# Kernel optimization log

Measured on AMD Instinct MI355X. Metric: run time of the kernel, lower is better.

Reference implementation:

```python
import jax, jax.numpy as jnp
import numpy as np

BN_EPS = 1e-5


def conv1x1(x, w, b):
    # x: (B,C,H,W), w: (O,C), b: (O,)
    return jnp.einsum('bchw,oc->bohw', x, w) + b[None, :, None, None]


def maxpool2(x):
    # 2x2 max pool, stride 2; H,W assumed even
    B, C, H, W = x.shape
    return x.reshape(B, C, H // 2, 2, W // 2, 2).max(axis=(3, 5))


def setup_inputs() -> dict:
    key = jax.random.key(0)
    ks = jax.random.split(key, 8)
    B, C, Ci, H, W = 8, 256, 128, 64, 64
    s_in = 1.0 / np.sqrt(C)   # kaiming-uniform-ish scale for 1x1 convs
    s_ci = 1.0 / np.sqrt(Ci)
    return {
        'x': jax.random.normal(ks[0], (B, C, H, W), jnp.float32),
        'theta_w': jax.random.normal(ks[1], (Ci, C), jnp.float32) * s_in,
        'theta_b': jnp.zeros((Ci,), jnp.float32),
        'phi_w': jax.random.normal(ks[2], (Ci, C), jnp.float32) * s_in,
        'phi_b': jnp.zeros((Ci,), jnp.float32),
        'g_w': jax.random.normal(ks[3], (Ci, C), jnp.float32) * s_in,
        'g_b': jnp.zeros((Ci,), jnp.float32),
        'W_w': jax.random.normal(ks[4], (C, Ci), jnp.float32) * s_ci,
        'W_b': jnp.zeros((C,), jnp.float32),
        'bn_gamma': jnp.ones((C,), jnp.float32),
        'bn_beta': jnp.zeros((C,), jnp.float32),
    }


def reference(x, theta_w, theta_b, phi_w, phi_b, g_w, g_b, W_w, W_b, bn_gamma, bn_beta):
    B, C, H, W = x.shape
    Ci = theta_w.shape[0]
    # 1x1 conv projections
    theta = conv1x1(x, theta_w, theta_b).reshape(B, Ci, H * W)           # (B,Ci,N)
    phi = maxpool2(conv1x1(x, phi_w, phi_b)).reshape(B, Ci, -1)          # (B,Ci,M)
    g = maxpool2(conv1x1(x, g_w, g_b)).reshape(B, Ci, -1)                # (B,Ci,M)
    # attention: softmax(theta^T phi) g^T
    attn = jax.nn.softmax(jnp.einsum('bcn,bcm->bnm', theta, phi), axis=-1)  # (B,N,M)
    y = jnp.einsum('bnm,bcm->bcn', attn, g).reshape(B, Ci, H, W)
    # output projection + BatchNorm2d (training-mode batch stats) + residual
    y = conv1x1(y, W_w, W_b)
    mean = y.mean(axis=(0, 2, 3))
    var = y.var(axis=(0, 2, 3))
    y = (y - mean[None, :, None, None]) * jax.lax.rsqrt(var + BN_EPS)[None, :, None, None]
    y = y * bn_gamma[None, :, None, None] + bn_beta[None, :, None, None]
    return x + y
```

## Files before the change

kernel.cpp:

```cpp
#include <hip/hip_runtime.h>

#define B_ 8
#define C_ 256
#define CI_ 128
#define N_ 4096
#define M_ 1024

typedef unsigned short u16;
typedef unsigned int u32;
typedef _Float16 f16x8 __attribute__((ext_vector_type(8)));
typedef _Float16 f16x4 __attribute__((ext_vector_type(4)));
typedef float f32x4 __attribute__((ext_vector_type(4)));
typedef u16 u16x4 __attribute__((ext_vector_type(4)));
typedef u16 u16x8 __attribute__((ext_vector_type(8)));

__device__ __forceinline__ u16 f2h(float f) {
    _Float16 h = (_Float16)f;
    u16 u;
    __builtin_memcpy(&u, &h, 2);
    return u;
}
__device__ __forceinline__ float h2f(u16 u) {
    _Float16 h;
    __builtin_memcpy(&h, &u, 2);
    return (float)h;
}
__device__ __forceinline__ f16x8 ldh8(const u16* p) {
    return *reinterpret_cast<const f16x8*>(p);
}
__device__ __forceinline__ f32x4 MFMAH(f16x8 a, f16x8 b, f32x4 c) {
    return __builtin_amdgcn_mfma_f32_16x16x32_f16(a, b, c, 0, 0, 0);
}
__device__ __forceinline__ f32x4 MFMA16(f16x4 a, f16x4 b, f32x4 c) {
    return __builtin_amdgcn_mfma_f32_16x16x16f16(a, b, c, 0, 0, 0);
}
__device__ __forceinline__ void gld16(const u16* g, u16* l) {
    __builtin_amdgcn_global_load_lds(
        (const __attribute__((address_space(1))) void*)g,
        (__attribute__((address_space(3))) void*)l, 16, 0, 0);
}


__global__ __launch_bounds__(256) void k_prep(
    const float* __restrict__ tw, const float* __restrict__ tb,
    const float* __restrict__ pw, const float* __restrict__ pb,
    const float* __restrict__ gw, const float* __restrict__ gb,
    const float* __restrict__ Ww,
    u16* __restrict__ wcf, float* __restrict__ bcat, u16* __restrict__ wwf) {
    int idx = blockIdx.x * 256 + threadIdx.x;
    if (idx < 384 * 256) {
        int r = idx >> 8, c = idx & 255;
        float v = (r < 128) ? tw[r * 256 + c]
                : (r < 256) ? pw[(r - 128) * 256 + c]
                            : gw[(r - 256) * 256 + c];
        size_t off = (size_t)((r >> 4) * 8 + (c >> 5)) * 512 +
                     (((c >> 3) & 3) * 16 + (r & 15)) * 8 + (c & 7);
        wcf[off] = f2h(v);
    } else if (idx < 384 * 256 + 256 * 128) {
        int k2 = idx - 384 * 256;
        int c = k2 >> 7, k = k2 & 127;
        size_t off = (size_t)((c >> 4) * 4 + (k >> 5)) * 512 +
                     (((k >> 3) & 3) * 16 + (c & 15)) * 8 + (k & 7);
        wwf[off] = f2h(Ww[k2]);
    } else if (idx < 384 * 256 + 256 * 128 + 384) {
        int r = idx - (384 * 256 + 256 * 128);
        bcat[r] = (r < 128) ? tb[r] : (r < 256) ? pb[r - 128] : gb[r - 256];
    }
}

__global__ __launch_bounds__(256) void k_tx(const float* __restrict__ x,
                                            u16* __restrict__ xbf) {
    int bid = blockIdx.x;
    int b = bid >> 8, rem = bid & 255, nt = rem >> 2, ct = rem & 3;
    int n0 = nt * 64, c0 = ct * 64;
    __shared__ u16 th_[64][66];
    int j = threadIdx.x & 63, i0 = threadIdx.x >> 6;
    for (int i = i0; i < 64; i += 4)
        th_[i][j] = f2h(x[((size_t)b * C_ + c0 + i) * N_ + n0 + j]);
    __syncthreads();
    int w = threadIdx.x >> 6, lane = threadIdx.x & 63;
    int l15 = lane & 15, g16 = lane >> 4;
    int s = w;
#pragma unroll
    for (int kk = 0; kk < 2; ++kk) {
        u16x8 hv;
#pragma unroll
        for (int e = 0; e < 8; ++e)
            hv[e] = th_[kk * 32 + g16 * 8 + e][s * 16 + l15];
        size_t off = ((size_t)(b * 256 + (n0 >> 4) + s) * 8 + (c0 >> 5) + kk) * 512 +
                     (size_t)lane * 8;
        *(u16x8*)&xbf[off] = hv;
    }
}

__global__ __launch_bounds__(256) void k_proj(
    const u16* __restrict__ wcf, const float* __restrict__ bcat,
    const u16* __restrict__ xbf,
    u16* __restrict__ thf, u16* __restrict__ ppf, u16* __restrict__ gpf) {
    int bid = blockIdx.x;
    int b = bid / 96, rem = bid % 96, rt = rem >> 5, nt = rem & 31;
    int tid = threadIdx.x;
    int w = tid >> 6, lane = tid & 63;
    int l15 = lane & 15, g16 = lane >> 4;
    int wr = (w >> 1) * 64, wc = (w & 1) * 64;
    int rbase = rt * 128 + wr, nbase = nt * 128 + wc;
    __shared__ u16 tl[128][132];
    f32x4 acc[4][4];
#pragma unroll
    for (int i = 0; i < 4; ++i)
#pragma unroll
        for (int j = 0; j < 4; ++j)
#pragma unroll
            for (int r = 0; r < 4; ++r) acc[i][j][r] = 0.f;
#pragma unroll
    for (int ks = 0; ks < 8; ++ks) {
        f16x8 a[4], bb[4];
#pragma unroll
        for (int i = 0; i < 4; ++i)
            a[i] = ldh8(&wcf[((size_t)((rbase >> 4) + i) * 8 + ks) * 512 + (size_t)lane * 8]);
#pragma unroll
        for (int j = 0; j < 4; ++j)
            bb[j] = ldh8(&xbf[((size_t)(b * 256 + (nbase >> 4) + j) * 8 + ks) * 512 +
                              (size_t)lane * 8]);
#pragma unroll
        for (int i = 0; i < 4; ++i)
#pragma unroll
            for (int j = 0; j < 4; ++j) acc[i][j] = MFMAH(a[i], bb[j], acc[i][j]);
    }
    if (rt == 0) {
#pragma unroll
        for (int i = 0; i < 4; ++i) {
            int lrow = wr + i * 16 + g16 * 4;
#pragma unroll
            for (int j = 0; j < 4; ++j) {
                u16x4 pk;
#pragma unroll
                for (int r = 0; r < 4; ++r)
                    pk[r] = f2h(acc[i][j][r] + bcat[lrow + r]);
                size_t off = ((size_t)(b * 256 + (nbase >> 4) + j) * 4 + (lrow >> 5)) * 512 +
                             (((lrow >> 3) & 3) * 16 + l15) * 8 + (lrow & 7);
                *reinterpret_cast<u16x4*>(&thf[off]) = pk;
            }
        }
    } else {
#pragma unroll
        for (int i = 0; i < 4; ++i) {
            int lrow = wr + i * 16 + g16 * 4;
#pragma unroll
            for (int j = 0; j < 4; ++j) {
                int n_loc = wc + j * 16 + l15;
                u16x4 pk;
#pragma unroll
                for (int r = 0; r < 4; ++r)
                    pk[r] = f2h(acc[i][j][r] + bcat[rt * 128 + lrow + r]);
                *reinterpret_cast<u16x4*>(&tl[n_loc][lrow]) = pk;
            }
        }
        __syncthreads();
        if (rt == 1) {
#pragma unroll
            for (int half = 0; half < 2; ++half) {
                int w2 = (tid >> 4) + half * 16;
                int c8 = tid & 15;
                u16x8 v0 = *(const u16x8*)&tl[2 * w2][c8 * 8];
                u16x8 v1 = *(const u16x8*)&tl[2 * w2 + 1][c8 * 8];
                u16x8 v2 = *(const u16x8*)&tl[64 + 2 * w2][c8 * 8];
                u16x8 v3 = *(const u16x8*)&tl[65 + 2 * w2][c8 * 8];
                u16x8 o;
#pragma unroll
                for (int e = 0; e < 8; ++e) {
                    float mx = fmaxf(fmaxf(h2f(v0[e]), h2f(v1[e])),
                                     fmaxf(h2f(v2[e]), h2f(v3[e])));
                    o[e] = f2h(mx);
                }
                size_t off = ((size_t)(((b * 32 + nt) * 2 + (w2 >> 4)) * 4 + (c8 >> 2)) * 64 +
                              (c8 & 3) * 16 + (w2 & 15)) * 8;
                *(u16x8*)&ppf[off] = o;
            }
        } else {
#pragma unroll
            for (int s = 0; s < 2; ++s) {
                int wg = (tid >> 7) + s * 2;
                int ci = tid & 127;
                u16x4 o0, o1;
#pragma unroll
                for (int e = 0; e < 4; ++e) {
                    int w2a = wg * 8 + e;
                    int w2b = wg * 8 + 4 + e;
                    float va = fmaxf(fmaxf(h2f(tl[2 * w2a][ci]), h2f(tl[2 * w2a + 1][ci])),
                                     fmaxf(h2f(tl[64 + 2 * w2a][ci]), h2f(tl[65 + 2 * w2a][ci])));
                    float vb = fmaxf(fmaxf(h2f(tl[2 * w2b][ci]), h2f(tl[2 * w2b + 1][ci])),
                                     fmaxf(h2f(tl[64 + 2 * w2b][ci]), h2f(tl[65 + 2 * w2b][ci])));
                    o0[e] = f2h(va);
                    o1[e] = f2h(vb);
                }
                size_t base = (size_t)(b * 32 + nt) * 4096 +
                              (size_t)(((wg >> 1) * 8) + (ci >> 4)) * 256 + (ci & 15) * 4;
                *(u16x4*)&gpf[base + (((wg * 2) & 3) * 64)] = o0;
                *(u16x4*)&gpf[base + (((wg * 2 + 1) & 3) * 64)] = o1;
            }
        }
    }
}

__global__ __launch_bounds__(256) void k_attn(
    const u16* __restrict__ thf, const u16* __restrict__ ppf,
    const u16* __restrict__ gpf, u16* __restrict__ ytf) {
    int bid = blockIdx.x;
    int b = bid & 7, nt = bid >> 3;
    int tid = threadIdx.x;
    int w = tid >> 6, lane = tid & 63;
    int l15 = lane & 15, g16 = lane >> 4;
    int n = nt * 64 + w * 16 + l15;
    int t16 = nt * 4 + w;
    __shared__ u16 kv[2][8192];

    f16x8 qf[4];
#pragma unroll
    for (int ks = 0; ks < 4; ++ks)
        qf[ks] = ldh8(&thf[((size_t)(b * 256 + t16) * 4 + ks) * 512 + (size_t)lane * 8]);

    f32x4 o[8];
#pragma unroll
    for (int ct = 0; ct < 8; ++ct)
#pragma unroll
        for (int rr = 0; rr < 4; ++rr) o[ct][rr] = 0.f;
    float mrun = -1e30f, lpart = 0.f;

    int soff = w * 512 + lane * 8;
    auto stage = [&](int bufidx, int itg) {
        const u16* ps = &ppf[(size_t)(b * 32 + itg) * 4096];
        const u16* gs = &gpf[(size_t)(b * 32 + itg) * 4096];
        u16* kb = &kv[bufidx][w * 512];
        gld16(ps + soff, kb);
        gld16(ps + 2048 + soff, kb + 2048);
        gld16(gs + soff, kb + 4096);
        gld16(gs + 2048 + soff, kb + 6144);
    };
    stage(0, 0);
    __syncthreads();
    int cur = 0;

    for (int it = 0; it < 32; ++it) {
        if (it < 31) stage(cur ^ 1, it + 1);
        f32x4 s0 = {0.f, 0.f, 0.f, 0.f}, s1 = {0.f, 0.f, 0.f, 0.f};
        __builtin_amdgcn_s_setprio(1);
#pragma unroll
        for (int ks = 0; ks < 4; ++ks) {
            f16x8 pa0 = ldh8(&kv[cur][ks * 512 + lane * 8]);
            f16x8 pa1 = ldh8(&kv[cur][(4 + ks) * 512 + lane * 8]);
            s0 = MFMAH(pa0, qf[ks], s0);
            s1 = MFMAH(pa1, qf[ks], s1);
        }
        __builtin_amdgcn_s_setprio(0);
        float pm8 = s0[0];
#pragma unroll
        for (int rr = 1; rr < 4; ++rr) pm8 = fmaxf(pm8, s0[rr]);
#pragma unroll
        for (int rr = 0; rr < 4; ++rr) pm8 = fmaxf(pm8, s1[rr]);
        if (__any(pm8 > mrun + 8.0f)) {
            float pm = fmaxf(pm8, __shfl_xor(pm8, 16));
            pm = fmaxf(pm, __shfl_xor(pm, 32));
            float mnew = fmaxf(mrun, pm);
            float sc = __expf(mrun - mnew);
#pragma unroll
            for (int ct = 0; ct < 8; ++ct)
#pragma unroll
                for (int rr = 0; rr < 4; ++rr) o[ct][rr] *= sc;
            lpart *= sc;
            mrun = mnew;
        }
        f16x4 pb0, pb1;
#pragma unroll
        for (int rr = 0; rr < 4; ++rr) {
            float p0 = __expf(s0[rr] - mrun);
            float p1 = __expf(s1[rr] - mrun);
            lpart += p0 + p1;
            pb0[rr] = (_Float16)p0;
            pb1[rr] = (_Float16)p1;
        }
        __builtin_amdgcn_s_setprio(1);
#pragma unroll
        for (int ct = 0; ct < 8; ++ct) {
            f16x4 g0 = *reinterpret_cast<const f16x4*>(&kv[cur][4096 + ct * 256 + lane * 4]);
            f16x4 g1 = *reinterpret_cast<const f16x4*>(&kv[cur][6144 + ct * 256 + lane * 4]);
            o[ct] = MFMA16(g0, pb0, o[ct]);
            o[ct] = MFMA16(g1, pb1, o[ct]);
        }
        __builtin_amdgcn_s_setprio(0);
        __syncthreads();
        cur ^= 1;
    }
    float lcol = lpart + __shfl_xor(lpart, 16);
    lcol += __shfl_xor(lcol, 32);
    float linv = 1.f / lcol;
    size_t obase = ((size_t)b * N_ + n) * CI_;
#pragma unroll
    for (int ct = 0; ct < 8; ++ct) {
        u16x4 pk;
#pragma unroll
        for (int rr = 0; rr < 4; ++rr) pk[rr] = f2h(o[ct][rr] * linv);
        *reinterpret_cast<u16x4*>(&ytf[obase + ct * 16 + g16 * 4]) = pk;
    }
}

__global__ __launch_bounds__(256) void k_wconv(
    const u16* __restrict__ wwf, const float* __restrict__ Wb,
    const u16* __restrict__ ytf, u16* __restrict__ z) {
    int bid = blockIdx.x;
    int b = bid >> 6, rem = bid & 63, ct2 = rem >> 5, nt = rem & 31;
    int w = threadIdx.x >> 6, lane = threadIdx.x & 63;
    int l15 = lane & 15, g16 = lane >> 4;
    int nbase = nt * 128 + (w >> 1) * 64;
    int cbase = ct2 * 128 + (w & 1) * 64;
    f32x4 acc[4][4];
#pragma unroll
    for (int i = 0; i < 4; ++i)
#pragma unroll
        for (int j = 0; j < 4; ++j)
#pragma unroll
            for (int r = 0; r < 4; ++r) acc[i][j][r] = 0.f;
#pragma unroll
    for (int ks = 0; ks < 4; ++ks) {
        f16x8 a[4], bb[4];
#pragma unroll
        for (int i = 0; i < 4; ++i) {
            int n = nbase + i * 16 + l15;
            a[i] = ldh8(&ytf[((size_t)b * N_ + n) * CI_ + ks * 32 + g16 * 8]);
        }
#pragma unroll
        for (int j = 0; j < 4; ++j)
            bb[j] = ldh8(&wwf[((size_t)((cbase >> 4) + j) * 4 + ks) * 512 + (size_t)lane * 8]);
#pragma unroll
        for (int i = 0; i < 4; ++i)
#pragma unroll
            for (int j = 0; j < 4; ++j) acc[i][j] = MFMAH(a[i], bb[j], acc[i][j]);
    }
#pragma unroll
    for (int j = 0; j < 4; ++j) {
        int ch = cbase + j * 16 + l15;
        float bias = Wb[ch];
        size_t rowbase = ((size_t)b * C_ + ch) * N_;
#pragma unroll
        for (int i = 0; i < 4; ++i) {
            u16x4 pk;
#pragma unroll
            for (int r = 0; r < 4; ++r) pk[r] = f2h(acc[i][j][r] + bias);
            *reinterpret_cast<u16x4*>(&z[rowbase + nbase + i * 16 + g16 * 4]) = pk;
        }
    }
}

__global__ __launch_bounds__(256) void k_stats(
    const u16* __restrict__ z, const float* __restrict__ gamma,
    const float* __restrict__ beta, float* __restrict__ bnp) {
    int c = blockIdx.x;
    int tid = threadIdx.x;
    float s = 0.f, q = 0.f;
#pragma unroll
    for (int b = 0; b < B_; ++b) {
        size_t base = ((size_t)b * C_ + c) * N_ + tid * 16;
        u16x8 v0 = *(const u16x8*)&z[base];
        u16x8 v1 = *(const u16x8*)&z[base + 8];
#pragma unroll
        for (int e = 0; e < 8; ++e) {
            float v = h2f(v0[e]);
            s += v;
            q += v * v;
            float u = h2f(v1[e]);
            s += u;
            q += u * u;
        }
    }
#pragma unroll
    for (int off = 1; off <= 32; off <<= 1) {
        s += __shfl_xor(s, off);
        q += __shfl_xor(q, off);
    }
    __shared__ float ss[4], qq[4];
    int w = tid >> 6;
    if ((tid & 63) == 0) {
        ss[w] = s;
        qq[w] = q;
    }
    __syncthreads();
    if (tid == 0) {
        s = ss[0] + ss[1] + ss[2] + ss[3];
        q = qq[0] + qq[1] + qq[2] + qq[3];
        const float inv_n = 1.f / 32768.f;
        float mean = s * inv_n;
        float var = q * inv_n - mean * mean;
        float sc = gamma[c] * rsqrtf(var + 1e-5f);
        bnp[c] = sc;
        bnp[256 + c] = beta[c] - mean * sc;
    }
}

__global__ __launch_bounds__(256) void k_final(
    const float* __restrict__ x, const u16* __restrict__ z,
    const float* __restrict__ bnp, float* __restrict__ out) {
    int i4 = blockIdx.x * 256 + threadIdx.x;
    size_t flat = (size_t)i4 * 4;
    int c = (int)((flat >> 12) & 255);
    float sc = bnp[c], sh = bnp[256 + c];
    float4 xx = *(const float4*)&x[flat];
    u16x4 zz = *(const u16x4*)&z[flat];
    float4 oo;
    oo.x = xx.x + h2f(zz[0]) * sc + sh;
    oo.y = xx.y + h2f(zz[1]) * sc + sh;
    oo.z = xx.z + h2f(zz[2]) * sc + sh;
    oo.w = xx.w + h2f(zz[3]) * sc + sh;
    *(float4*)&out[flat] = oo;
}

extern "C" void kernel_launch(void* const* d_in, const int* in_sizes, int n_in,
                              void* d_out, int out_size, void* d_ws, size_t ws_size,
                              hipStream_t stream) {
    const float* x     = (const float*)d_in[0];
    const float* tw    = (const float*)d_in[1];
    const float* tb    = (const float*)d_in[2];
    const float* pw    = (const float*)d_in[3];
    const float* pb    = (const float*)d_in[4];
    const float* gw    = (const float*)d_in[5];
    const float* gb    = (const float*)d_in[6];
    const float* Ww    = (const float*)d_in[7];
    const float* Wb    = (const float*)d_in[8];
    const float* gamma = (const float*)d_in[9];
    const float* beta  = (const float*)d_in[10];
    float* out = (float*)d_out;

    char* p = (char*)d_ws;
    auto alloc = [&](size_t bytes) {
        char* r = p;
        p += (bytes + 255) & ~(size_t)255;
        return r;
    };
    u16* xbf   = (u16*)alloc((size_t)B_ * N_ * C_ * 2);
    u16* thf   = (u16*)alloc((size_t)B_ * N_ * CI_ * 2);
    u16* ppf   = (u16*)alloc((size_t)B_ * M_ * CI_ * 2);
    u16* gpf   = (u16*)alloc((size_t)B_ * M_ * CI_ * 2);
    u16* ytf   = (u16*)alloc((size_t)B_ * N_ * CI_ * 2);
    u16* z     = (u16*)alloc((size_t)B_ * C_ * N_ * 2);
    u16* wcf   = (u16*)alloc(384 * 256 * 2);
    u16* wwf   = (u16*)alloc(256 * 128 * 2);
    float* bcat = (float*)alloc(384 * 4);
    float* bnp  = (float*)alloc(512 * 4);

    k_prep<<<514, 256, 0, stream>>>(tw, tb, pw, pb, gw, gb, Ww, wcf, bcat, wwf);
    k_tx<<<2048, 256, 0, stream>>>(x, xbf);
    k_proj<<<768, 256, 0, stream>>>(wcf, bcat, xbf, thf, ppf, gpf);
    k_attn<<<512, 256, 0, stream>>>(thf, ppf, gpf, ytf);
    k_wconv<<<512, 256, 0, stream>>>(wwf, Wb, ytf, z);
    k_stats<<<256, 256, 0, stream>>>(z, gamma, beta, bnp);
    k_final<<<8192, 256, 0, stream>>>(x, z, bnp, out);
}
```

Measured before the change: 97.86 us.

## Fuse BN statistics into output conv epilogue and vectorize transpose loads

Batch-norm sum and sum-of-squares are now accumulated in the k_wconv epilogue from fp32 values and combined with per-channel atomics. This removes the separate k_stats pass that re-read z from memory. A tiny k_meanvar kernel turns the sums into scale and shift, and two memsets clear the accumulators each call. The k_tx transpose also switches to float4 global loads with packed fp16 stores to shared memory, at the cost of extra launches for the memsets and atomic contention.

Result: slower. 111.8 us (+14.2%).

```diff
diff --git a/kernel.cpp b/kernel.cpp
--- a/kernel.cpp
+++ b/kernel.cpp
@@ -74,11 +74,21 @@
     int b = bid >> 8, rem = bid & 255, nt = rem >> 2, ct = rem & 3;
     int n0 = nt * 64, c0 = ct * 64;
     __shared__ u16 th_[64][66];
-    int j = threadIdx.x & 63, i0 = threadIdx.x >> 6;
-    for (int i = i0; i < 64; i += 4)
-        th_[i][j] = f2h(x[((size_t)b * C_ + c0 + i) * N_ + n0 + j]);
+    int t = threadIdx.x;
+    int i0 = t >> 4, jg = t & 15;
+#pragma unroll
+    for (int pass = 0; pass < 4; ++pass) {
+        int i = i0 + pass * 16;
+        float4 v = *(const float4*)&x[((size_t)b * C_ + c0 + i) * N_ + n0 + jg * 4];
+        u16x4 pk;
+        pk[0] = f2h(v.x);
+        pk[1] = f2h(v.y);
+        pk[2] = f2h(v.z);
+        pk[3] = f2h(v.w);
+        *reinterpret_cast<u16x4*>(&th_[i][jg * 4]) = pk;
+    }
     __syncthreads();
-    int w = threadIdx.x >> 6, lane = threadIdx.x & 63;
+    int w = t >> 6, lane = t & 63;
     int l15 = lane & 15, g16 = lane >> 4;
     int s = w;
 #pragma unroll
@@ -306,7 +316,8 @@
 
 __global__ __launch_bounds__(256) void k_wconv(
     const u16* __restrict__ wwf, const float* __restrict__ Wb,
-    const u16* __restrict__ ytf, u16* __restrict__ z) {
+    const u16* __restrict__ ytf, u16* __restrict__ z,
+    float* __restrict__ ssum, float* __restrict__ ssq) {
     int bid = blockIdx.x;
     int b = bid >> 6, rem = bid & 63, ct2 = rem >> 5, nt = rem & 31;
     int w = threadIdx.x >> 6, lane = threadIdx.x & 63;
@@ -341,59 +352,41 @@
         int ch = cbase + j * 16 + l15;
         float bias = Wb[ch];
         size_t rowbase = ((size_t)b * C_ + ch) * N_;
+        float s = 0.f, q = 0.f;
 #pragma unroll
         for (int i = 0; i < 4; ++i) {
             u16x4 pk;
 #pragma unroll
-            for (int r = 0; r < 4; ++r) pk[r] = f2h(acc[i][j][r] + bias);
+            for (int r = 0; r < 4; ++r) {
+                float v = acc[i][j][r] + bias;
+                pk[r] = f2h(v);
+                s += v;
+                q += v * v;
+            }
             *reinterpret_cast<u16x4*>(&z[rowbase + nbase + i * 16 + g16 * 4]) = pk;
         }
-    }
-}
-
-__global__ __launch_bounds__(256) void k_stats(
-    const u16* __restrict__ z, const float* __restrict__ gamma,
-    const float* __restrict__ beta, float* __restrict__ bnp) {
-    int c = blockIdx.x;
-    int tid = threadIdx.x;
-    float s = 0.f, q = 0.f;
-#pragma unroll
-    for (int b = 0; b < B_; ++b) {
-        size_t base = ((size_t)b * C_ + c) * N_ + tid * 16;
-        u16x8 v0 = *(const u16x8*)&z[base];
-        u16x8 v1 = *(const u16x8*)&z[base + 8];
-#pragma unroll
-        for (int e = 0; e < 8; ++e) {
-            float v = h2f(v0[e]);
-            s += v;
-            q += v * v;
-            float u = h2f(v1[e]);
-            s += u;
-            q += u * u;
-        }
-    }
-#pragma unroll
-    for (int off = 1; off <= 32; off <<= 1) {
-        s += __shfl_xor(s, off);
-        q += __shfl_xor(q, off);
-    }
-    __shared__ float ss[4], qq[4];
-    int w = tid >> 6;
-    if ((tid & 63) == 0) {
-        ss[w] = s;
-        qq[w] = q;
-    }
-    __syncthreads();
-    if (tid == 0) {
-        s = ss[0] + ss[1] + ss[2] + ss[3];
-        q = qq[0] + qq[1] + qq[2] + qq[3];
-        const float inv_n = 1.f / 32768.f;
-        float mean = s * inv_n;
-        float var = q * inv_n - mean * mean;
-        float sc = gamma[c] * rsqrtf(var + 1e-5f);
-        bnp[c] = sc;
-        bnp[256 + c] = beta[c] - mean * sc;
-    }
+        s += __shfl_xor(s, 16);
+        q += __shfl_xor(q, 16);
+        s += __shfl_xor(s, 32);
+        q += __shfl_xor(q, 32);
+        if (g16 == 0) {
+            atomicAdd(&ssum[ch], s);
+            atomicAdd(&ssq[ch], q);
+        }
+    }
+}
+
+__global__ __launch_bounds__(256) void k_meanvar(
+    const float* __restrict__ ssum, const float* __restrict__ ssq,
+    const float* __restrict__ gamma, const float* __restrict__ beta,
+    float* __restrict__ bnp) {
+    int c = threadIdx.x;
+    const float inv_n = 1.f / 32768.f;
+    float mean = ssum[c] * inv_n;
+    float var = ssq[c] * inv_n - mean * mean;
+    float sc = gamma[c] * rsqrtf(var + 1e-5f);
+    bnp[c] = sc;
+    bnp[256 + c] = beta[c] - mean * sc;
 }
 
 __global__ __launch_bounds__(256) void k_final(
@@ -444,13 +437,18 @@
     u16* wcf   = (u16*)alloc(384 * 256 * 2);
     u16* wwf   = (u16*)alloc(256 * 128 * 2);
     float* bcat = (float*)alloc(384 * 4);
+    float* ssum = (float*)alloc(256 * 4);
+    float* ssq  = (float*)alloc(256 * 4);
     float* bnp  = (float*)alloc(512 * 4);
+
+    (void)hipMemsetAsync(ssum, 0, 256 * 4, stream);
+    (void)hipMemsetAsync(ssq, 0, 256 * 4, stream);
 
     k_prep<<<514, 256, 0, stream>>>(tw, tb, pw, pb, gw, gb, Ww, wcf, bcat, wwf);
     k_tx<<<2048, 256, 0, stream>>>(x, xbf);
     k_proj<<<768, 256, 0, stream>>>(wcf, bcat, xbf, thf, ppf, gpf);
     k_attn<<<512, 256, 0, stream>>>(thf, ppf, gpf, ytf);
-    k_wconv<<<512, 256, 0, stream>>>(wwf, Wb, ytf, z);
-    k_stats<<<256, 256, 0, stream>>>(z, gamma, beta, bnp);
+    k_wconv<<<512, 256, 0, stream>>>(wwf, Wb, ytf, z, ssum, ssq);
+    k_meanvar<<<1, 256, 0, stream>>>(ssum, ssq, gamma, beta, bnp);
     k_final<<<8192, 256, 0, stream>>>(x, z, bnp, out);
 }
```
